# Kernel optimization log

Hardware: AMD Instinct MI355X
Metric: run time of the kernel (lower is better)

The kernel has to match this reference:

```python
import jax, jax.numpy as jnp
import numpy as np

B, IN, OUT = 4096, 1024, 1024
HALF_PI = np.pi / 2.0
TWO_PI = 2.0 * np.pi
# cyclic control-point index table per quadrant (from the torch module)
CPI = jnp.array([[3, 0, 1, 2], [0, 1, 2, 3], [1, 2, 3, 0], [2, 3, 0, 1]], dtype=jnp.int32)
# Catmull-Rom cubic spline basis (4 control points, [t^3,t^2,t,1] monomials)
BASIS = np.array([[-0.5, 1.5, -1.5, 0.5],
                  [1.0, -2.5, 2.0, -0.5],
                  [-0.5, 0.0, 0.5, 0.0],
                  [0.0, 1.0, 0.0, 0.0]], dtype=np.float32)


def setup_inputs() -> dict:
    key = jax.random.key(0)
    k_x, k_p, k_w, k_b = jax.random.split(key, 4)
    x = jax.random.normal(k_x, (B, IN), dtype=jnp.float32)
    phase = jax.random.uniform(k_p, (B,), dtype=jnp.float32) * TWO_PI
    # kaiming_uniform_(a=sqrt(5)) on each (OUT, IN) slice -> bound = 1/sqrt(fan_in)
    bound = 1.0 / np.sqrt(IN)
    weights = jax.random.uniform(k_w, (4, OUT, IN), dtype=jnp.float32, minval=-bound, maxval=bound)
    biases = jax.random.uniform(k_b, (4, OUT), dtype=jnp.float32, minval=-bound, maxval=bound)
    basis = jnp.asarray(BASIS)
    return {"input": x, "phase": phase, "weights": weights, "biases": biases, "basis": basis}


def reference(input, phase, weights, biases, basis):
    # quadrant index q in {0,1,2,3}; same selection as the nested torch.where chain
    q = jnp.clip(jnp.floor(phase / HALF_PI).astype(jnp.int32), 0, 3)          # (B,)
    t = phase / HALF_PI - q.astype(phase.dtype)                                # (B,), in [0,1)
    tt = jnp.stack([t ** 3, t ** 2, t, jnp.ones_like(t)], axis=-1)             # (B,4)
    coeffs = tt @ basis                                                        # (B,4) spline coeffs
    idx = CPI[q]                                                               # (B,4) control-point ids
    # Instead of materializing per-sample (B,OUT,IN) weights, contract input against
    # all 4 control-point matrices (same math: w_b = sum_k c_k W_{idx_k}).
    z = jnp.einsum('bi,coi->bco', input, weights)                              # (B,4,OUT)
    zg = jnp.take_along_axis(z, idx[:, :, None], axis=1)                       # (B,4,OUT)
    bg = biases[idx]                                                           # (B,4,OUT)
    return jnp.einsum('bk,bko->bo', coeffs, zg + bg)                           # (B,OUT)
```

## Files before the change

### kernel.cpp

```cpp
#include <hip/hip_runtime.h>
#include <stdint.h>

#define BATCH   4096
#define IN_DIM  1024
#define OUT_DIM 1024

typedef __bf16 bf16x8 __attribute__((ext_vector_type(8)));
typedef float  f32x4  __attribute__((ext_vector_type(4)));

__device__ __forceinline__ uint16_t f2bf(float f) {
    union { float f; uint32_t u; } v; v.f = f;
    uint32_t u = v.u;
    uint32_t r = (u + 0x7FFFu + ((u >> 16) & 1u)) >> 16;
    return (uint16_t)r;
}

__global__ __launch_bounds__(256) void prep(
    const float* __restrict__ x, const float* __restrict__ phase,
    const float* __restrict__ basis, const float* __restrict__ W,
    uint16_t* __restrict__ xb, uint16_t* __restrict__ Wb,
    float* __restrict__ alphaWS)
{
    const int bid = blockIdx.x;
    const int tid = threadIdx.x;

    if (bid < BATCH) {
        const int b = bid;
        const float HALF_PI = 1.5707963267948966f;
        float s  = phase[b] / HALF_PI;
        int   q  = (int)floorf(s);
        q = q < 0 ? 0 : (q > 3 ? 3 : q);
        float t  = s - (float)q;
        float t2 = t * t, t3 = t2 * t;

        float coef[4];
#pragma unroll
        for (int j = 0; j < 4; ++j)
            coef[j] = t3 * basis[j] + t2 * basis[4 + j] + t * basis[8 + j] + basis[12 + j];

        if (tid < 4) alphaWS[b * 4 + tid] = coef[(tid - q + 1) & 3];

        float4 xv = ((const float4*)(x + (size_t)b * IN_DIM))[tid];
        ushort4 o;
        o.x = f2bf(xv.x); o.y = f2bf(xv.y); o.z = f2bf(xv.z); o.w = f2bf(xv.w);
        ((ushort4*)(xb + (size_t)b * IN_DIM))[tid] = o;
    } else {
        const int j = bid - BATCH;
        float4 wv = ((const float4*)W)[j * 256 + tid];
        ushort4 o;
        o.x = f2bf(wv.x); o.y = f2bf(wv.y); o.z = f2bf(wv.z); o.w = f2bf(wv.w);
        ((ushort4*)Wb)[j * 256 + tid] = o;
    }
}

__global__ __launch_bounds__(256, 4) void gemm_split(
    const uint16_t* __restrict__ xb, const uint16_t* __restrict__ Wb,
    float* __restrict__ P0, float* __restrict__ P123)
{
    __shared__ uint16_t As[128 * 64];
    __shared__ uint16_t Bs[128 * 64];

    const int tid  = threadIdx.x;
    const int lane = tid & 63;
    const int wid  = tid >> 6;
    const int wm   = wid >> 1;
    const int wn   = wid & 1;
    const int tileM = blockIdx.x * 128;
    const int tileN = blockIdx.y * 128;
    const int c     = blockIdx.z;

    f32x4 acc[4][4];
#pragma unroll
    for (int mi = 0; mi < 4; ++mi)
#pragma unroll
        for (int ni = 0; ni < 4; ++ni)
            acc[mi][ni] = (f32x4){0.f, 0.f, 0.f, 0.f};

    const int srow = lane >> 3;
    const int gchunk = ((lane & 7) ^ srow) * 8;

    const uint16_t* Ag = xb + (size_t)tileM * 1024;
    const uint16_t* Bg = Wb + ((size_t)c << 20) + (size_t)tileN * 1024;

    const int quad = lane >> 4;
    const int l7   = lane & 7;

    for (int kt = 0; kt < 16; ++kt) {
        const int k0 = kt * 64;
#pragma unroll
        for (int j = 0; j < 4; ++j) {
            const int s = wid * 4 + j;
            const uint16_t* ga = Ag + (size_t)(s * 8 + srow) * 1024 + k0 + gchunk;
            __builtin_amdgcn_global_load_lds(
                (const __attribute__((address_space(1))) void*)ga,
                (__attribute__((address_space(3))) void*)(As + s * 512), 16, 0, 0);
            const uint16_t* gb = Bg + (size_t)(s * 8 + srow) * 1024 + k0 + gchunk;
            __builtin_amdgcn_global_load_lds(
                (const __attribute__((address_space(1))) void*)gb,
                (__attribute__((address_space(3))) void*)(Bs + s * 512), 16, 0, 0);
        }
        __syncthreads();

#pragma unroll
        for (int ks = 0; ks < 2; ++ks) {
            bf16x8 af[4], bfr[4];
#pragma unroll
            for (int mi = 0; mi < 4; ++mi) {
                const int row = wm * 64 + mi * 16 + (lane & 15);
                const int ch  = (ks * 4 + quad) ^ l7;
                af[mi] = *(const bf16x8*)(As + row * 64 + ch * 8);
            }
#pragma unroll
            for (int ni = 0; ni < 4; ++ni) {
                const int row = wn * 64 + ni * 16 + (lane & 15);
                const int ch  = (ks * 4 + quad) ^ l7;
                bfr[ni] = *(const bf16x8*)(Bs + row * 64 + ch * 8);
            }
#pragma unroll
            for (int mi = 0; mi < 4; ++mi)
#pragma unroll
                for (int ni = 0; ni < 4; ++ni)
                    acc[mi][ni] = __builtin_amdgcn_mfma_f32_16x16x32_bf16(
                        af[mi], bfr[ni], acc[mi][ni], 0, 0, 0);
        }
        __syncthreads();
    }

    float* Pc = (c == 0) ? P0 : (P123 + (size_t)(c - 1) * (BATCH * (size_t)OUT_DIM));
    const int col0 = tileN + wn * 64 + (lane & 15);
#pragma unroll
    for (int mi = 0; mi < 4; ++mi) {
#pragma unroll
        for (int r = 0; r < 4; ++r) {
            const int m = tileM + wm * 64 + mi * 16 + quad * 4 + r;
#pragma unroll
            for (int ni = 0; ni < 4; ++ni)
                Pc[(size_t)m * OUT_DIM + col0 + ni * 16] = acc[mi][ni][r];
        }
    }
}

__global__ __launch_bounds__(256) void reduce_k(
    const float* __restrict__ P123, const float* __restrict__ alphaWS,
    const float* __restrict__ biases, float* __restrict__ out)
{
    const int m = blockIdx.x;
    const int t = threadIdx.x;
    const size_t stride = (size_t)BATCH * OUT_DIM;

    const float4 al = *(const float4*)(alphaWS + 4 * m);
    const float4 p0 = ((const float4*)(out + (size_t)m * OUT_DIM))[t];
    const float4 p1 = ((const float4*)(P123 + 0 * stride + (size_t)m * OUT_DIM))[t];
    const float4 p2 = ((const float4*)(P123 + 1 * stride + (size_t)m * OUT_DIM))[t];
    const float4 p3 = ((const float4*)(P123 + 2 * stride + (size_t)m * OUT_DIM))[t];
    const float4 b0 = ((const float4*)(biases + 0 * OUT_DIM))[t];
    const float4 b1 = ((const float4*)(biases + 1 * OUT_DIM))[t];
    const float4 b2 = ((const float4*)(biases + 2 * OUT_DIM))[t];
    const float4 b3 = ((const float4*)(biases + 3 * OUT_DIM))[t];

    float4 r;
    r.x = al.x * (p0.x + b0.x) + al.y * (p1.x + b1.x) + al.z * (p2.x + b2.x) + al.w * (p3.x + b3.x);
    r.y = al.x * (p0.y + b0.y) + al.y * (p1.y + b1.y) + al.z * (p2.y + b2.y) + al.w * (p3.y + b3.y);
    r.z = al.x * (p0.z + b0.z) + al.y * (p1.z + b1.z) + al.z * (p2.z + b2.z) + al.w * (p3.z + b3.z);
    r.w = al.x * (p0.w + b0.w) + al.y * (p1.w + b1.w) + al.z * (p2.w + b2.w) + al.w * (p3.w + b3.w);
    ((float4*)(out + (size_t)m * OUT_DIM))[t] = r;
}

extern "C" void kernel_launch(void* const* d_in, const int* in_sizes, int n_in,
                              void* d_out, int out_size, void* d_ws, size_t ws_size,
                              hipStream_t stream)
{
    const float* x       = (const float*)d_in[0];
    const float* phase   = (const float*)d_in[1];
    const float* weights = (const float*)d_in[2];
    const float* biases  = (const float*)d_in[3];
    const float* basis   = (const float*)d_in[4];
    float* out = (float*)d_out;

    uint16_t* xb = (uint16_t*)d_ws;
    uint16_t* Wb = xb + (size_t)BATCH * IN_DIM;
    float* alphaWS = (float*)(Wb + (size_t)4 * OUT_DIM * IN_DIM);
    float* P123 = alphaWS + (size_t)BATCH * 4;

    prep<<<2 * BATCH, 256, 0, stream>>>(x, phase, basis, weights, xb, Wb, alphaWS);

    dim3 grid(BATCH / 128, OUT_DIM / 128, 4);
    gemm_split<<<grid, 256, 0, stream>>>(xb, Wb, out, P123);

    reduce_k<<<BATCH, 256, 0, stream>>>(P123, alphaWS, biases, out);
}
```

Before: 133.8 us.

## Fuse reduction into GEMM epilogue via atomic adds and bias init in prep

The prep kernel now writes the alpha-weighted bias sum into the output. Each of the four control-point GEMMs scales its accumulator by the per-row alpha and atomically adds it into the output. This removes the fp32 partial-product buffers and the separate reduce kernel, cutting a large write/read round trip and one launch. In exchange it relies on global fp32 atomics, whose summation order is nondeterministic and whose scalar RMW throughput may limit the epilogue.

```diff
diff --git a/kernel.cpp b/kernel.cpp
--- a/kernel.cpp
+++ b/kernel.cpp
@@ -18,8 +18,9 @@
 __global__ __launch_bounds__(256) void prep(
     const float* __restrict__ x, const float* __restrict__ phase,
     const float* __restrict__ basis, const float* __restrict__ W,
+    const float* __restrict__ biases,
     uint16_t* __restrict__ xb, uint16_t* __restrict__ Wb,
-    float* __restrict__ alphaWS)
+    float* __restrict__ alphaWS, float* __restrict__ out)
 {
     const int bid = blockIdx.x;
     const int tid = threadIdx.x;
@@ -38,12 +39,26 @@
         for (int j = 0; j < 4; ++j)
             coef[j] = t3 * basis[j] + t2 * basis[4 + j] + t * basis[8 + j] + basis[12 + j];
 
-        if (tid < 4) alphaWS[b * 4 + tid] = coef[(tid - q + 1) & 3];
+        float al[4];
+#pragma unroll
+        for (int c = 0; c < 4; ++c) al[c] = coef[(c - q + 1) & 3];
+        if (tid < 4) alphaWS[b * 4 + tid] = al[tid];
 
         float4 xv = ((const float4*)(x + (size_t)b * IN_DIM))[tid];
         ushort4 o;
         o.x = f2bf(xv.x); o.y = f2bf(xv.y); o.z = f2bf(xv.z); o.w = f2bf(xv.w);
         ((ushort4*)(xb + (size_t)b * IN_DIM))[tid] = o;
+
+        float4 b0 = ((const float4*)(biases + 0 * OUT_DIM))[tid];
+        float4 b1 = ((const float4*)(biases + 1 * OUT_DIM))[tid];
+        float4 b2 = ((const float4*)(biases + 2 * OUT_DIM))[tid];
+        float4 b3 = ((const float4*)(biases + 3 * OUT_DIM))[tid];
+        float4 r;
+        r.x = al[0] * b0.x + al[1] * b1.x + al[2] * b2.x + al[3] * b3.x;
+        r.y = al[0] * b0.y + al[1] * b1.y + al[2] * b2.y + al[3] * b3.y;
+        r.z = al[0] * b0.z + al[1] * b1.z + al[2] * b2.z + al[3] * b3.z;
+        r.w = al[0] * b0.w + al[1] * b1.w + al[2] * b2.w + al[3] * b3.w;
+        ((float4*)(out + (size_t)b * OUT_DIM))[tid] = r;
     } else {
         const int j = bid - BATCH;
         float4 wv = ((const float4*)W)[j * 256 + tid];
@@ -55,7 +70,7 @@
 
 __global__ __launch_bounds__(256, 4) void gemm_split(
     const uint16_t* __restrict__ xb, const uint16_t* __restrict__ Wb,
-    float* __restrict__ P0, float* __restrict__ P123)
+    const float* __restrict__ alphaWS, float* __restrict__ out)
 {
     __shared__ uint16_t As[128 * 64];
     __shared__ uint16_t Bs[128 * 64];
@@ -126,44 +141,19 @@
         __syncthreads();
     }
 
-    float* Pc = (c == 0) ? P0 : (P123 + (size_t)(c - 1) * (BATCH * (size_t)OUT_DIM));
     const int col0 = tileN + wn * 64 + (lane & 15);
 #pragma unroll
     for (int mi = 0; mi < 4; ++mi) {
 #pragma unroll
         for (int r = 0; r < 4; ++r) {
             const int m = tileM + wm * 64 + mi * 16 + quad * 4 + r;
+            const float a = alphaWS[4 * m + c];
+            float* orow = out + (size_t)m * OUT_DIM + col0;
 #pragma unroll
             for (int ni = 0; ni < 4; ++ni)
-                Pc[(size_t)m * OUT_DIM + col0 + ni * 16] = acc[mi][ni][r];
+                unsafeAtomicAdd(orow + ni * 16, a * acc[mi][ni][r]);
         }
     }
-}
-
-__global__ __launch_bounds__(256) void reduce_k(
-    const float* __restrict__ P123, const float* __restrict__ alphaWS,
-    const float* __restrict__ biases, float* __restrict__ out)
-{
-    const int m = blockIdx.x;
-    const int t = threadIdx.x;
-    const size_t stride = (size_t)BATCH * OUT_DIM;
-
-    const float4 al = *(const float4*)(alphaWS + 4 * m);
-    const float4 p0 = ((const float4*)(out + (size_t)m * OUT_DIM))[t];
-    const float4 p1 = ((const float4*)(P123 + 0 * stride + (size_t)m * OUT_DIM))[t];
-    const float4 p2 = ((const float4*)(P123 + 1 * stride + (size_t)m * OUT_DIM))[t];
-    const float4 p3 = ((const float4*)(P123 + 2 * stride + (size_t)m * OUT_DIM))[t];
-    const float4 b0 = ((const float4*)(biases + 0 * OUT_DIM))[t];
-    const float4 b1 = ((const float4*)(biases + 1 * OUT_DIM))[t];
-    const float4 b2 = ((const float4*)(biases + 2 * OUT_DIM))[t];
-    const float4 b3 = ((const float4*)(biases + 3 * OUT_DIM))[t];
-
-    float4 r;
-    r.x = al.x * (p0.x + b0.x) + al.y * (p1.x + b1.x) + al.z * (p2.x + b2.x) + al.w * (p3.x + b3.x);
-    r.y = al.x * (p0.y + b0.y) + al.y * (p1.y + b1.y) + al.z * (p2.y + b2.y) + al.w * (p3.y + b3.y);
-    r.z = al.x * (p0.z + b0.z) + al.y * (p1.z + b1.z) + al.z * (p2.z + b2.z) + al.w * (p3.z + b3.z);
-    r.w = al.x * (p0.w + b0.w) + al.y * (p1.w + b1.w) + al.z * (p2.w + b2.w) + al.w * (p3.w + b3.w);
-    ((float4*)(out + (size_t)m * OUT_DIM))[t] = r;
 }
 
 extern "C" void kernel_launch(void* const* d_in, const int* in_sizes, int n_in,
@@ -180,12 +170,10 @@
     uint16_t* xb = (uint16_t*)d_ws;
     uint16_t* Wb = xb + (size_t)BATCH * IN_DIM;
     float* alphaWS = (float*)(Wb + (size_t)4 * OUT_DIM * IN_DIM);
-    float* P123 = alphaWS + (size_t)BATCH * 4;
 
-    prep<<<2 * BATCH, 256, 0, stream>>>(x, phase, basis, weights, xb, Wb, alphaWS);
+    prep<<<2 * BATCH, 256, 0, stream>>>(x, phase, basis, weights, biases,
+                                        xb, Wb, alphaWS, out);
 
     dim3 grid(BATCH / 128, OUT_DIM / 128, 4);
-    gemm_split<<<grid, 256, 0, stream>>>(xb, Wb, out, P123);
-
-    reduce_k<<<BATCH, 256, 0, stream>>>(P123, alphaWS, biases, out);
+    gemm_split<<<grid, 256, 0, stream>>>(xb, Wb, alphaWS, out);
 }
```

Result: slower. 161.8 us (+20.9%).
